# Performance work log

Measured on AMD Instinct MI355X. Metric: run time of the kernel, lower is better.

## Reference

```python
import jax, jax.numpy as jnp
import numpy as np

N_HEAD = 16

def setup_inputs() -> dict:
    key = jax.random.key(0)
    k1, k2, k3 = jax.random.split(key, 3)
    B, T, C = 4, 2048, 1024
    x = jax.random.normal(k1, (B, T, C), dtype=jnp.float32)
    w_attn = jax.random.normal(k2, (C, 3 * C), dtype=jnp.float32) * 0.02
    w_o = jax.random.normal(k3, (C, C), dtype=jnp.float32) * 0.02
    return {"x": x, "w_attn": w_attn, "w_o": w_o}

def reference(x, w_attn, w_o):
    B, T, C = x.shape
    H = N_HEAD
    hs = C // H
    qkv = x @ w_attn  # [B,T,3C]
    q, k, v = jnp.split(qkv, 3, axis=-1)
    # [B,H,T,hs]
    q = q.reshape(B, T, H, hs).transpose(0, 2, 1, 3)
    k = k.reshape(B, T, H, hs).transpose(0, 2, 1, 3)
    v = v.reshape(B, T, H, hs).transpose(0, 2, 1, 3)
    att = jnp.einsum('bhqd,bhkd->bhqk', q, k) * (1.0 / np.sqrt(hs).astype(np.float32))
    causal = jnp.tril(jnp.ones((T, T), dtype=bool))
    att = jnp.where(causal[None, None], att, jnp.float32(-jnp.inf))
    att = jax.nn.softmax(att, axis=-1)
    y = jnp.einsum('bhqk,bhkd->bhqd', att, v)
    y = y.transpose(0, 2, 1, 3).reshape(B, T, C)
    return y @ w_o
```

## Files before the change

### kernel.cpp

```cpp
#include <hip/hip_runtime.h>

typedef unsigned short u16;
typedef unsigned int u32;
typedef __attribute__((ext_vector_type(8))) __bf16 bf16x8;
typedef __attribute__((ext_vector_type(4))) float f32x4;
typedef __attribute__((ext_vector_type(8))) unsigned short u16x8;
typedef __attribute__((ext_vector_type(4))) unsigned int u32x4;

typedef const __attribute__((address_space(1))) u32 gu32;
typedef __attribute__((address_space(3))) u32 lu32;

__device__ __forceinline__ u16 f2b(float f) {
  u32 u = __builtin_bit_cast(u32, f);
  u32 r = u + 0x7fffu + ((u >> 16) & 1u);
  return (u16)(r >> 16);
}

__device__ __forceinline__ u32 pk2(float lo, float hi) {
  u32 d;
  asm("v_cvt_pk_bf16_f32 %0, %1, %2" : "=v"(d) : "v"(lo), "v"(hi));
  return d;
}

__device__ __forceinline__ bf16x8 pack8(f32x4 a, f32x4 b) {
  u32x4 u;
  u[0] = pk2(a[0], a[1]);
  u[1] = pk2(a[2], a[3]);
  u[2] = pk2(b[0], b[1]);
  u[3] = pk2(b[2], b[3]);
  return __builtin_bit_cast(bf16x8, u);
}

__device__ __forceinline__ bf16x8 ld8(const u16* p) {
  return __builtin_bit_cast(bf16x8, *(const u16x8*)p);
}

__device__ __forceinline__ void gll16(const void* g, void* l) {
  __builtin_amdgcn_global_load_lds((gu32*)g, (lu32*)l, 16, 0, 0);
}

__device__ __forceinline__ f32x4 mfma16(bf16x8 a, bf16x8 b, f32x4 c) {
  return __builtin_amdgcn_mfma_f32_16x16x32_bf16(a, b, c, 0, 0, 0);
}

__global__ void k_cvt(const float* __restrict__ in, u16* __restrict__ out, int n4) {
  int i = blockIdx.x * blockDim.x + threadIdx.x;
  int stride = gridDim.x * blockDim.x;
  for (int idx = i; idx < n4; idx += stride) {
    float4 v = ((const float4*)in)[idx];
    u32 lo = (u32)f2b(v.x) | ((u32)f2b(v.y) << 16);
    u32 hi = (u32)f2b(v.z) | ((u32)f2b(v.w) << 16);
    ((uint2*)out)[idx] = make_uint2(lo, hi);
  }
}

__global__ void k_tr(const float* __restrict__ in, u16* __restrict__ out, int R, int C) {
  __shared__ u16 tile[32][33];
  int bx = blockIdx.x * 32;
  int by = blockIdx.y * 32;
  int tx = threadIdx.x, ty = threadIdx.y;
#pragma unroll
  for (int i = 0; i < 32; i += 8)
    tile[ty + i][tx] = f2b(in[(size_t)(by + ty + i) * C + bx + tx]);
  __syncthreads();
#pragma unroll
  for (int i = 0; i < 32; i += 8)
    out[(size_t)(bx + ty + i) * R + by + tx] = tile[tx][ty + i];
}

template <int EPI>
__global__ __launch_bounds__(256) void k_gemm(const u16* __restrict__ A,
                                              const u16* __restrict__ B,
                                              void* __restrict__ Cp) {
  const int K = 1024;
  const int NT = 32;
  __shared__ __align__(16) u16 As[2][128 * 32];
  __shared__ __align__(16) u16 Bs[2][128 * 32];
  int tid = threadIdx.x;
  int lane = tid & 63, wid = tid >> 6;
  int wr = wid >> 1, wc = wid & 1;
  int m0 = blockIdx.y * 128, n0 = blockIdx.x * 128;
  int r = lane & 15, qq = lane >> 4;

  const u16* Ag0 = A + (size_t)(m0 + wid * 32 + (lane >> 2)) * K + (lane & 3) * 8;
  const u16* Bg0 = B + (size_t)(n0 + wid * 32 + (lane >> 2)) * K + (lane & 3) * 8;
  int sl0 = (wid * 32) * 32;
  int sl1 = (wid * 32 + 16) * 32;

#define GSTAGE(buf, k0)                          \
  do {                                           \
    gll16(Ag0 + (k0), &As[buf][sl0]);            \
    gll16(Ag0 + 16 * K + (k0), &As[buf][sl1]);   \
    gll16(Bg0 + (k0), &Bs[buf][sl0]);            \
    gll16(Bg0 + 16 * K + (k0), &Bs[buf][sl1]);   \
  } while (0)

  f32x4 acc[4][4] = {};

  GSTAGE(0, 0);
  GSTAGE(1, 32);

  for (int kt = 0; kt < NT; ++kt) {
    int cur = kt & 1;
    if (kt + 1 < NT)
      asm volatile("s_waitcnt vmcnt(4)" ::: "memory");
    else
      asm volatile("s_waitcnt vmcnt(0)" ::: "memory");
    __builtin_amdgcn_s_barrier();

    bf16x8 af[4], bfr[4];
#pragma unroll
    for (int m = 0; m < 4; ++m)
      af[m] = ld8(&As[cur][(wr * 64 + m * 16 + r) * 32 + qq * 8]);
#pragma unroll
    for (int n = 0; n < 4; ++n)
      bfr[n] = ld8(&Bs[cur][(wc * 64 + n * 16 + r) * 32 + qq * 8]);
    asm volatile("s_waitcnt lgkmcnt(0)" ::: "memory");
    __builtin_amdgcn_sched_barrier(0);
    __builtin_amdgcn_s_barrier();

    if (kt + 2 < NT) GSTAGE(cur, (kt + 2) * 32);

#pragma unroll
    for (int m = 0; m < 4; ++m)
#pragma unroll
      for (int n = 0; n < 4; ++n) acc[m][n] = mfma16(af[m], bfr[n], acc[m][n]);
  }
#undef GSTAGE

  if constexpr (EPI == 0) {
    u16* qkv = (u16*)Cp;
#pragma unroll
    for (int m = 0; m < 4; ++m) {
      int gr = m0 + wr * 64 + m * 16 + qq * 4;
      int b = gr >> 11, t0 = gr & 2047;
#pragma unroll
      for (int n = 0; n < 4; ++n) {
        int gc = n0 + wc * 64 + n * 16 + r;
        int which = gc >> 10, rem = gc & 1023;
        int hh = rem >> 6, d = rem & 63;
        if (which == 2) {
          u16* dst = qkv + (size_t)2 * 8388608u +
                     ((size_t)((b * 16 + hh) * 64 + d)) * 2048 + t0;
          u32 p0 = pk2(acc[m][n][0], acc[m][n][1]);
          u32 p1 = pk2(acc[m][n][2], acc[m][n][3]);
          *(uint2*)dst = make_uint2(p0, p1);
        } else {
          float sc = (which == 0) ? 0.18033688011112042f : 1.0f;
          u16* dst = qkv + (size_t)which * 8388608u +
                     ((size_t)((b * 16 + hh) * 2048 + t0)) * 64 + d;
#pragma unroll
          for (int i = 0; i < 4; ++i) dst[(size_t)i * 64] = f2b(acc[m][n][i] * sc);
        }
      }
    }
  } else {
    float* out = (float*)Cp;
#pragma unroll
    for (int m = 0; m < 4; ++m) {
      int gr = m0 + wr * 64 + m * 16 + qq * 4;
#pragma unroll
      for (int n = 0; n < 4; ++n) {
        int gc = n0 + wc * 64 + n * 16 + r;
#pragma unroll
        for (int i = 0; i < 4; ++i) out[(size_t)(gr + i) * 1024 + gc] = acc[m][n][i];
      }
    }
  }
}

__global__ __launch_bounds__(256) void k_attn(const u16* __restrict__ Qm,
                                              const u16* __restrict__ Km,
                                              const u16* __restrict__ VTm,
                                              u16* __restrict__ Y) {
  int bi = blockIdx.x;
  int x = bi >> 6;
  int bh = bi & 63;
  int b = bh >> 4, h = bh & 15;
  int qb0 = (15 - x) * 128;
  int tid = threadIdx.x, lane = tid & 63, w = tid >> 6;
  int r = lane & 15, qq = lane >> 4;
  const size_t base = (size_t)bh * (2048 * 64);
  int q0w = qb0 + w * 32;

  __shared__ __align__(16) u16 Kt[2][64 * 64];
  __shared__ __align__(16) u16 Vt[2][64 * 64];

  bf16x8 qf[2][2];
#pragma unroll
  for (int m = 0; m < 2; ++m)
#pragma unroll
    for (int kc = 0; kc < 2; ++kc)
      qf[m][kc] = ld8(Qm + base + (size_t)(q0w + m * 16 + r) * 64 + kc * 32 + qq * 8);

  f32x4 acc[2][4] = {};
  float m_run[2] = {-1e30f, -1e30f};
  float l_run[2] = {0.f, 0.f};
  int ntwg = (qb0 >> 6) + 2;

  int srow = lane >> 3;
  int kch0 = (lane & 7) ^ (srow & 3);
  int kch1 = (lane & 7) ^ ((srow & 3) | 4);
  int vch = (lane & 7) ^ srow;
  const u16* Kg = Km + base;
  const u16* Vg = VTm + base;

  int ar = 8 * (r >> 2) + (r & 3);
  int fkl = (r & 3) | (((r >> 2) & 1) << 2);
  int ks0 = ((qq ^ fkl)) * 8, ks1 = ((qq ^ fkl) ^ 4) * 8;
  int fvl = r & 7;
  int vs0 = ((qq ^ fvl)) * 8, vs1 = ((qq ^ fvl) ^ 4) * 8;

#define STAGE(buf, j0n)                                                                 \
  do {                                                                                  \
    gll16(Kg + (size_t)((j0n) + w * 16 + srow) * 64 + kch0 * 8,                         \
          &Kt[buf][(w * 16) * 64]);                                                     \
    gll16(Kg + (size_t)((j0n) + w * 16 + 8 + srow) * 64 + kch1 * 8,                     \
          &Kt[buf][(w * 16 + 8) * 64]);                                                 \
    gll16(Vg + (size_t)(w * 16 + srow) * 2048 + (j0n) + vch * 8,                        \
          &Vt[buf][(w * 16) * 64]);                                                     \
    gll16(Vg + (size_t)(w * 16 + 8 + srow) * 2048 + (j0n) + vch * 8,                    \
          &Vt[buf][(w * 16 + 8) * 64]);                                                 \
  } while (0)

  STAGE(0, 0);
  __syncthreads();

  for (int it = 0; it < ntwg; ++it) {
    int j0 = it << 6;
    int cur = it & 1;
    bool active = (j0 <= q0w + 31);
    f32x4 s[4][2];
    bf16x8 vfr[4][2];

    if (active) {
      __builtin_amdgcn_s_setprio(1);
#pragma unroll
      for (int nt = 0; nt < 4; ++nt) {
        int knt = 32 * (nt >> 1) + 4 * (nt & 1);
        const u16* kb_ = &Kt[cur][(knt + ar) * 64];
        bf16x8 k0 = ld8(kb_ + ks0);
        bf16x8 k1 = ld8(kb_ + ks1);
#pragma unroll
        for (int m = 0; m < 2; ++m) {
          f32x4 z = {};
          s[nt][m] = mfma16(k1, qf[m][1], mfma16(k0, qf[m][0], z));
        }
      }
#pragma unroll
      for (int n = 0; n < 4; ++n) {
        const u16* vb_ = &Vt[cur][(n * 16 + r) * 64];
        vfr[n][0] = ld8(vb_ + vs0);
        vfr[n][1] = ld8(vb_ + vs1);
      }
      __builtin_amdgcn_s_setprio(0);
    }

    if (it + 1 < ntwg) STAGE(cur ^ 1, j0 + 64);

    if (active) {
      bool nm = (j0 + 63 > q0w);
      if (nm) {
#pragma unroll
        for (int nt = 0; nt < 4; ++nt) {
          int kb = j0 + 32 * (nt >> 1) + 4 * (nt & 1) + 8 * qq;
#pragma unroll
          for (int m = 0; m < 2; ++m) {
            int qg = q0w + m * 16 + r;
#pragma unroll
            for (int i = 0; i < 4; ++i)
              s[nt][m][i] = (kb + i <= qg) ? s[nt][m][i] : -1e30f;
          }
        }
      }

      float tm[2];
#pragma unroll
      for (int m = 0; m < 2; ++m) {
        float t0 = fmaxf(fmaxf(s[0][m][0], s[0][m][1]), fmaxf(s[0][m][2], s[0][m][3]));
        float t1 = fmaxf(fmaxf(s[1][m][0], s[1][m][1]), fmaxf(s[1][m][2], s[1][m][3]));
        float t2 = fmaxf(fmaxf(s[2][m][0], s[2][m][1]), fmaxf(s[2][m][2], s[2][m][3]));
        float t3 = fmaxf(fmaxf(s[3][m][0], s[3][m][1]), fmaxf(s[3][m][2], s[3][m][3]));
        float t = fmaxf(fmaxf(t0, t1), fmaxf(t2, t3));
        t = fmaxf(t, __shfl_xor(t, 16));
        t = fmaxf(t, __shfl_xor(t, 32));
        tm[m] = t;
      }

      int grow = (tm[0] > m_run[0]) | (tm[1] > m_run[1]);
      if (__any(grow)) {
#pragma unroll
        for (int m = 0; m < 2; ++m) {
          float mn = fmaxf(m_run[m], tm[m]);
          float corr = __builtin_amdgcn_exp2f(m_run[m] - mn);
          m_run[m] = mn;
          l_run[m] *= corr;
#pragma unroll
          for (int i = 0; i < 4; ++i) {
            float c = __shfl(corr, qq * 4 + i);
#pragma unroll
            for (int n = 0; n < 4; ++n) acc[m][n][i] *= c;
          }
        }
      }

#pragma unroll
      for (int m = 0; m < 2; ++m) {
        float ls = 0.f;
#pragma unroll
        for (int nt = 0; nt < 4; ++nt)
#pragma unroll
          for (int i = 0; i < 4; ++i) {
            float e = __builtin_amdgcn_exp2f(s[nt][m][i] - m_run[m]);
            s[nt][m][i] = e;
            ls += e;
          }
        l_run[m] += ls;
      }

      __builtin_amdgcn_s_setprio(1);
#pragma unroll
      for (int m = 0; m < 2; ++m) {
        bf16x8 pa0 = pack8(s[0][m], s[1][m]);
        bf16x8 pa1 = pack8(s[2][m], s[3][m]);
#pragma unroll
        for (int n = 0; n < 4; ++n) acc[m][n] = mfma16(pa0, vfr[n][0], acc[m][n]);
#pragma unroll
        for (int n = 0; n < 4; ++n) acc[m][n] = mfma16(pa1, vfr[n][1], acc[m][n]);
      }
      __builtin_amdgcn_s_setprio(0);
    }

    __syncthreads();
  }
#undef STAGE

  float li[2][4];
#pragma unroll
  for (int m = 0; m < 2; ++m) {
    float l = l_run[m];
    l += __shfl_xor(l, 16);
    l += __shfl_xor(l, 32);
    float inv = 1.0f / l;
#pragma unroll
    for (int i = 0; i < 4; ++i) li[m][i] = __shfl(inv, qq * 4 + i);
  }
#pragma unroll
  for (int m = 0; m < 2; ++m)
#pragma unroll
    for (int n = 0; n < 4; ++n)
#pragma unroll
      for (int i = 0; i < 4; ++i)
        Y[((size_t)(b * 2048 + q0w + m * 16 + qq * 4 + i)) * 1024 + h * 64 + n * 16 + r] =
            f2b(acc[m][n][i] * li[m][i]);
}

extern "C" void kernel_launch(void* const* d_in, const int* in_sizes, int n_in,
                              void* d_out, int out_size, void* d_ws, size_t ws_size,
                              hipStream_t stream) {
  const float* x = (const float*)d_in[0];
  const float* w_attn = (const float*)d_in[1];
  const float* w_o = (const float*)d_in[2];
  float* out = (float*)d_out;

  char* ws = (char*)d_ws;
  u16* xb = (u16*)(ws + 0);
  u16* watT = (u16*)(ws + 16777216);
  u16* woT = (u16*)(ws + 23068672);
  u16* qb = (u16*)(ws + 25165824);
  u16* kb = (u16*)(ws + 41943040);
  u16* vb = (u16*)(ws + 58720256);
  u16* yb = (u16*)(ws + 75497472);

  k_cvt<<<2048, 256, 0, stream>>>(x, xb, 8192 * 1024 / 4);
  k_tr<<<dim3(3072 / 32, 1024 / 32), dim3(32, 8), 0, stream>>>(w_attn, watT, 1024, 3072);
  k_tr<<<dim3(1024 / 32, 1024 / 32), dim3(32, 8), 0, stream>>>(w_o, woT, 1024, 1024);
  k_gemm<0><<<dim3(24, 64), 256, 0, stream>>>(xb, watT, (void*)qb);
  k_attn<<<dim3(1024), 256, 0, stream>>>(qb, kb, vb, yb);
  k_gemm<1><<<dim3(8, 64), 256, 0, stream>>>(yb, woT, (void*)out);
}
```

Measured before the change: 187.6 us.

## Swizzle GEMM LDS tiles and give attention warps 64 query rows each

```diff
diff --git a/kernel.cpp b/kernel.cpp
--- a/kernel.cpp
+++ b/kernel.cpp
@@ -82,10 +82,12 @@
   int m0 = blockIdx.y * 128, n0 = blockIdx.x * 128;
   int r = lane & 15, qq = lane >> 4;
 
-  const u16* Ag0 = A + (size_t)(m0 + wid * 32 + (lane >> 2)) * K + (lane & 3) * 8;
-  const u16* Bg0 = B + (size_t)(n0 + wid * 32 + (lane >> 2)) * K + (lane & 3) * 8;
+  int schunk = (lane & 3) ^ ((lane >> 3) & 3);
+  const u16* Ag0 = A + (size_t)(m0 + wid * 32 + (lane >> 2)) * K + schunk * 8;
+  const u16* Bg0 = B + (size_t)(n0 + wid * 32 + (lane >> 2)) * K + schunk * 8;
   int sl0 = (wid * 32) * 32;
   int sl1 = (wid * 32 + 16) * 32;
+  int rsw = (qq ^ ((r >> 1) & 3)) * 8;
 
 #define GSTAGE(buf, k0)                          \
   do {                                           \
@@ -111,10 +113,10 @@
     bf16x8 af[4], bfr[4];
 #pragma unroll
     for (int m = 0; m < 4; ++m)
-      af[m] = ld8(&As[cur][(wr * 64 + m * 16 + r) * 32 + qq * 8]);
+      af[m] = ld8(&As[cur][(wr * 64 + m * 16 + r) * 32 + rsw]);
 #pragma unroll
     for (int n = 0; n < 4; ++n)
-      bfr[n] = ld8(&Bs[cur][(wc * 64 + n * 16 + r) * 32 + qq * 8]);
+      bfr[n] = ld8(&Bs[cur][(wc * 64 + n * 16 + r) * 32 + rsw]);
     asm volatile("s_waitcnt lgkmcnt(0)" ::: "memory");
     __builtin_amdgcn_sched_barrier(0);
     __builtin_amdgcn_s_barrier();
@@ -169,7 +171,7 @@
   }
 }
 
-__global__ __launch_bounds__(256) void k_attn(const u16* __restrict__ Qm,
+__global__ __launch_bounds__(128) void k_attn(const u16* __restrict__ Qm,
                                               const u16* __restrict__ Km,
                                               const u16* __restrict__ VTm,
                                               u16* __restrict__ Y) {
@@ -181,26 +183,26 @@
   int tid = threadIdx.x, lane = tid & 63, w = tid >> 6;
   int r = lane & 15, qq = lane >> 4;
   const size_t base = (size_t)bh * (2048 * 64);
-  int q0w = qb0 + w * 32;
+  int q0w = qb0 + w * 64;
 
   __shared__ __align__(16) u16 Kt[2][64 * 64];
   __shared__ __align__(16) u16 Vt[2][64 * 64];
 
-  bf16x8 qf[2][2];
-#pragma unroll
-  for (int m = 0; m < 2; ++m)
+  bf16x8 qf[4][2];
+#pragma unroll
+  for (int m = 0; m < 4; ++m)
 #pragma unroll
     for (int kc = 0; kc < 2; ++kc)
       qf[m][kc] = ld8(Qm + base + (size_t)(q0w + m * 16 + r) * 64 + kc * 32 + qq * 8);
 
-  f32x4 acc[2][4] = {};
-  float m_run[2] = {-1e30f, -1e30f};
-  float l_run[2] = {0.f, 0.f};
+  f32x4 acc[4][4] = {};
+  float m_run[4] = {-1e30f, -1e30f, -1e30f, -1e30f};
+  float l_run[4] = {0.f, 0.f, 0.f, 0.f};
   int ntwg = (qb0 >> 6) + 2;
 
   int srow = lane >> 3;
-  int kch0 = (lane & 7) ^ (srow & 3);
-  int kch1 = (lane & 7) ^ ((srow & 3) | 4);
+  int kchA = (lane & 7) ^ (srow & 3);
+  int kchB = kchA ^ 4;
   int vch = (lane & 7) ^ srow;
   const u16* Kg = Km + base;
   const u16* Vg = VTm + base;
@@ -211,16 +213,24 @@
   int fvl = r & 7;
   int vs0 = ((qq ^ fvl)) * 8, vs1 = ((qq ^ fvl) ^ 4) * 8;
 
-#define STAGE(buf, j0n)                                                                 \
-  do {                                                                                  \
-    gll16(Kg + (size_t)((j0n) + w * 16 + srow) * 64 + kch0 * 8,                         \
-          &Kt[buf][(w * 16) * 64]);                                                     \
-    gll16(Kg + (size_t)((j0n) + w * 16 + 8 + srow) * 64 + kch1 * 8,                     \
-          &Kt[buf][(w * 16 + 8) * 64]);                                                 \
-    gll16(Vg + (size_t)(w * 16 + srow) * 2048 + (j0n) + vch * 8,                        \
-          &Vt[buf][(w * 16) * 64]);                                                     \
-    gll16(Vg + (size_t)(w * 16 + 8 + srow) * 2048 + (j0n) + vch * 8,                    \
-          &Vt[buf][(w * 16 + 8) * 64]);                                                 \
+#define STAGE(buf, j0n)                                                             \
+  do {                                                                              \
+    gll16(Kg + (size_t)((j0n) + w * 32 + srow) * 64 + kchA * 8,                     \
+          &Kt[buf][(w * 32) * 64]);                                                 \
+    gll16(Kg + (size_t)((j0n) + w * 32 + 8 + srow) * 64 + kchB * 8,                 \
+          &Kt[buf][(w * 32 + 8) * 64]);                                             \
+    gll16(Kg + (size_t)((j0n) + w * 32 + 16 + srow) * 64 + kchA * 8,                \
+          &Kt[buf][(w * 32 + 16) * 64]);                                            \
+    gll16(Kg + (size_t)((j0n) + w * 32 + 24 + srow) * 64 + kchB * 8,                \
+          &Kt[buf][(w * 32 + 24) * 64]);                                            \
+    gll16(Vg + (size_t)(w * 32 + srow) * 2048 + (j0n) + vch * 8,                    \
+          &Vt[buf][(w * 32) * 64]);                                                 \
+    gll16(Vg + (size_t)(w * 32 + 8 + srow) * 2048 + (j0n) + vch * 8,                \
+          &Vt[buf][(w * 32 + 8) * 64]);                                             \
+    gll16(Vg + (size_t)(w * 32 + 16 + srow) * 2048 + (j0n) + vch * 8,               \
+          &Vt[buf][(w * 32 + 16) * 64]);                                            \
+    gll16(Vg + (size_t)(w * 32 + 24 + srow) * 2048 + (j0n) + vch * 8,               \
+          &Vt[buf][(w * 32 + 24) * 64]);                                            \
   } while (0)
 
   STAGE(0, 0);
@@ -229,8 +239,8 @@
   for (int it = 0; it < ntwg; ++it) {
     int j0 = it << 6;
     int cur = it & 1;
-    bool active = (j0 <= q0w + 31);
-    f32x4 s[4][2];
+    bool active = (j0 <= q0w + 63);
+    f32x4 s[4][4];
     bf16x8 vfr[4][2];
 
     if (active) {
@@ -242,7 +252,7 @@
         bf16x8 k0 = ld8(kb_ + ks0);
         bf16x8 k1 = ld8(kb_ + ks1);
 #pragma unroll
-        for (int m = 0; m < 2; ++m) {
+        for (int m = 0; m < 4; ++m) {
           f32x4 z = {};
           s[nt][m] = mfma16(k1, qf[m][1], mfma16(k0, qf[m][0], z));
         }
@@ -265,7 +275,7 @@
         for (int nt = 0; nt < 4; ++nt) {
           int kb = j0 + 32 * (nt >> 1) + 4 * (nt & 1) + 8 * qq;
 #pragma unroll
-          for (int m = 0; m < 2; ++m) {
+          for (int m = 0; m < 4; ++m) {
             int qg = q0w + m * 16 + r;
 #pragma unroll
             for (int i = 0; i < 4; ++i)
@@ -274,9 +284,9 @@
         }
       }
 
-      float tm[2];
-#pragma unroll
-      for (int m = 0; m < 2; ++m) {
+      float tm[4];
+#pragma unroll
+      for (int m = 0; m < 4; ++m) {
         float t0 = fmaxf(fmaxf(s[0][m][0], s[0][m][1]), fmaxf(s[0][m][2], s[0][m][3]));
         float t1 = fmaxf(fmaxf(s[1][m][0], s[1][m][1]), fmaxf(s[1][m][2], s[1][m][3]));
         float t2 = fmaxf(fmaxf(s[2][m][0], s[2][m][1]), fmaxf(s[2][m][2], s[2][m][3]));
@@ -287,10 +297,11 @@
         tm[m] = t;
       }
 
-      int grow = (tm[0] > m_run[0]) | (tm[1] > m_run[1]);
+      int grow = (tm[0] > m_run[0]) | (tm[1] > m_run[1]) | (tm[2] > m_run[2]) |
+                 (tm[3] > m_run[3]);
       if (__any(grow)) {
 #pragma unroll
-        for (int m = 0; m < 2; ++m) {
+        for (int m = 0; m < 4; ++m) {
           float mn = fmaxf(m_run[m], tm[m]);
           float corr = __builtin_amdgcn_exp2f(m_run[m] - mn);
           m_run[m] = mn;
@@ -305,7 +316,7 @@
       }
 
 #pragma unroll
-      for (int m = 0; m < 2; ++m) {
+      for (int m = 0; m < 4; ++m) {
         float ls = 0.f;
 #pragma unroll
         for (int nt = 0; nt < 4; ++nt)
@@ -320,7 +331,7 @@
 
       __builtin_amdgcn_s_setprio(1);
 #pragma unroll
-      for (int m = 0; m < 2; ++m) {
+      for (int m = 0; m < 4; ++m) {
         bf16x8 pa0 = pack8(s[0][m], s[1][m]);
         bf16x8 pa1 = pack8(s[2][m], s[3][m]);
 #pragma unroll
@@ -335,9 +346,9 @@
   }
 #undef STAGE
 
-  float li[2][4];
-#pragma unroll
-  for (int m = 0; m < 2; ++m) {
+  float li[4][4];
+#pragma unroll
+  for (int m = 0; m < 4; ++m) {
     float l = l_run[m];
     l += __shfl_xor(l, 16);
     l += __shfl_xor(l, 32);
@@ -346,7 +357,7 @@
     for (int i = 0; i < 4; ++i) li[m][i] = __shfl(inv, qq * 4 + i);
   }
 #pragma unroll
-  for (int m = 0; m < 2; ++m)
+  for (int m = 0; m < 4; ++m)
 #pragma unroll
     for (int n = 0; n < 4; ++n)
 #pragma unroll
@@ -376,6 +387,6 @@
   k_tr<<<dim3(3072 / 32, 1024 / 32), dim3(32, 8), 0, stream>>>(w_attn, watT, 1024, 3072);
   k_tr<<<dim3(1024 / 32, 1024 / 32), dim3(32, 8), 0, stream>>>(w_o, woT, 1024, 1024);
   k_gemm<0><<<dim3(24, 64), 256, 0, stream>>>(xb, watT, (void*)qb);
-  k_attn<<<dim3(1024), 256, 0, stream>>>(qb, kb, vb, yb);
+  k_attn<<<dim3(1024), 128, 0, stream>>>(qb, kb, vb, yb);
   k_gemm<1><<<dim3(8, 64), 256, 0, stream>>>(yb, woT, (void*)out);
 }
```

Result: slower. 204.1 us (+8.8%).
